# Optimization experiments

Measured on AMD Instinct MI355X. Metric: run time of the kernel, lower is better.

## Reference

```python
import jax, jax.numpy as jnp
import numpy as np

NUM_HEADS = 8
EMBED_DIM = 128
HEAD_DIM = EMBED_DIM // NUM_HEADS  # 16
NB_FEATURES = EMBED_DIM            # 128
EPS = 1e-4


def _make_projection(nb_rows, nb_cols, rng):
    # gaussian_orthogonal_random_matrix with scaling=0
    blocks = []
    for _ in range(nb_rows // nb_cols):
        q, _ = np.linalg.qr(rng.standard_normal((nb_cols, nb_cols)))
        blocks.append(q.T)
    rem = nb_rows - (nb_rows // nb_cols) * nb_cols
    if rem > 0:
        q, _ = np.linalg.qr(rng.standard_normal((nb_cols, nb_cols)))
        blocks.append(q.T[:rem])
    final = np.concatenate(blocks, axis=0)
    mult = np.linalg.norm(rng.standard_normal((nb_rows, nb_cols)), axis=1)
    return (mult[:, None] * final).astype(np.float32)


def setup_inputs() -> dict:
    key = jax.random.key(0)
    ks = jax.random.split(key, 7)
    R, C, E = 8, 2048, EMBED_DIM
    s = 1.0 / np.sqrt(E)
    x = jax.random.normal(ks[0], (R, C, E), dtype=jnp.float32)
    Wq = jax.random.uniform(ks[1], (E, E), jnp.float32, -s, s)
    bq = jax.random.uniform(ks[2], (E,), jnp.float32, -s, s)
    Wk = jax.random.uniform(ks[3], (E, E), jnp.float32, -s, s)
    bk = jax.random.uniform(ks[4], (E,), jnp.float32, -s, s)
    Wv = jax.random.uniform(ks[5], (E, E), jnp.float32, -s, s)
    bv = jax.random.uniform(ks[6], (E,), jnp.float32, -s, s)
    proj = jnp.asarray(_make_projection(NB_FEATURES, HEAD_DIM, np.random.default_rng(0)))
    return {"x": x, "Wq": Wq, "bq": bq, "Wk": Wk, "bk": bk, "Wv": Wv, "bv": bv, "proj": proj}


def _softmax_kernel(data, proj, is_query):
    # data: (R, h, n, d); proj: (F, d)
    d = data.shape[-1]
    normalizer = d ** (-0.25)
    ratio = proj.shape[0] ** (-0.5)
    data_dash = jnp.einsum('rhnd,jd->rhnj', normalizer * data, proj)  # (R,h,n,F)
    diag = jnp.sum(data * data, axis=-1, keepdims=True) * 0.5 * normalizer ** 2
    if is_query:
        m = jnp.max(data_dash, axis=-1, keepdims=True)
    else:
        m = jnp.max(data_dash, axis=(-1, -2), keepdims=True)
    return ratio * (jnp.exp(data_dash - diag - m) + EPS)


def reference(x, Wq, bq, Wk, bk, Wv, bv, proj):
    R, C, E = x.shape
    h, hd = NUM_HEADS, HEAD_DIM

    def proj_heads(W, b):
        y = jnp.einsum('rce,fe->rcf', x, W) + b
        return y.reshape(R, C, h, hd).transpose(0, 2, 1, 3)  # (R,h,C,hd)

    q = _softmax_kernel(proj_heads(Wq, bq), proj, is_query=True)   # (R,h,C,F)
    k = _softmax_kernel(proj_heads(Wk, bk), proj, is_query=False)  # (R,h,C,F)
    v = proj_heads(Wv, bv)                                          # (R,h,C,hd)

    # fold batch (R) into the feature dim: (h, C, R*F) / (h, C, R*hd)
    qf = q.transpose(1, 2, 0, 3).reshape(h, C, R * NB_FEATURES)
    kf = k.transpose(1, 2, 0, 3).reshape(h, C, R * NB_FEATURES)
    vf = v.transpose(1, 2, 0, 3).reshape(h, C, R * hd)

    k_sum = kf.sum(axis=-2)                                   # (h, D)
    D_inv = 1.0 / jnp.einsum('hnd,hd->hn', qf, k_sum)         # (h, C)
    context = jnp.einsum('hnd,hne->hde', kf, vf)              # (h, D, Ev)
    out = jnp.einsum('hde,hnd,hn->hne', context, qf, D_inv)   # (h, C, R*hd)

    out = out.reshape(h, C, R, hd).transpose(2, 1, 0, 3).reshape(R, C, E)
    attn = jnp.einsum('hqf,hkf->hqk', qf, kf)                 # (h, C, C)
    return out, attn
```

## Files before the change

kernel.cpp:

```cpp
#include <hip/hip_runtime.h>
#include <hip/hip_bf16.h>
#include <stdint.h>

typedef __bf16 bf16x8 __attribute__((ext_vector_type(8)));
typedef __bf16 bf16x4 __attribute__((ext_vector_type(4)));
typedef float  f32x4  __attribute__((ext_vector_type(4)));

#define RATIO 0.08838834764831845f
#define EPSV  1e-4f

#define GLOBAL_AS __attribute__((address_space(1)))
#define LDS_AS    __attribute__((address_space(3)))

static __device__ __forceinline__ void gload16(const void* g, void* l) {
  __builtin_amdgcn_global_load_lds((GLOBAL_AS const void*)g, (LDS_AS void*)l, 16, 0, 0);
}

static constexpr size_t OFF_XB    = 0;
static constexpr size_t OFF_WCAT  = OFF_XB    + 4194304;
static constexpr size_t OFF_MQ    = OFF_WCAT  + 98304;
static constexpr size_t OFF_MK    = OFF_MQ    + 262144;
static constexpr size_t OFF_BCAT  = OFF_MK    + 262144;
static constexpr size_t OFF_BQF   = OFF_BCAT  + 2048;
static constexpr size_t OFF_BKF   = OFF_BQF   + 4096;
static constexpr size_t OFF_Y     = OFF_BKF   + 4096;
static constexpr size_t OFF_QF    = OFF_Y     + 25165824;
static constexpr size_t OFF_KF    = OFF_QF    + 33554432;
static constexpr size_t OFF_KFT   = OFF_KF    + 33554432;
static constexpr size_t OFF_VFT   = OFF_KFT   + 33554432;
static constexpr size_t OFF_KPART = OFF_VFT   + 4194304;
static constexpr size_t OFF_KMAX  = OFF_KPART + 4096;
static constexpr size_t OFF_KSPART= OFF_KMAX  + 1024;
static constexpr size_t OFF_DPART = OFF_KSPART+ 524288;
static constexpr size_t OFF_CTXP  = OFF_DPART + 524288;
static constexpr size_t OFF_CTXT  = OFF_CTXP  + 16777216;
static constexpr size_t WS_NEED   = OFF_CTXT  + 2097152;

static __device__ __forceinline__ void gemm_core(
    const __hip_bfloat16* __restrict__ A, const __hip_bfloat16* __restrict__ B,
    int lda, int ldb, int K, int tm, int tn,
    __bf16* As, __bf16* Bs, f32x4 acc[4][4]) {
  const int t    = threadIdx.x;
  const int w    = t >> 6;
  const int lane = t & 63;
  const int m_off = (w >> 1) << 6;
  const int n_off = (w & 1) << 6;
  const int r0 = t >> 2;
  const int kk = (t & 3) << 3;
  char* Asb = (char*)As + (w << 10);
  char* Bsb = (char*)Bs + (w << 10);
  const int frow = lane & 15;
  const int koff = (lane >> 4) << 3;
  for (int k0 = 0; k0 < K; k0 += 32) {
    const __hip_bfloat16* Ag = A + (size_t)(tm + r0) * lda + (k0 + kk);
    const __hip_bfloat16* Bg = B + (size_t)(tn + r0) * ldb + (k0 + kk);
    gload16(Ag, Asb);
    gload16(Ag + (size_t)64 * lda, Asb + 4096);
    gload16(Bg, Bsb);
    gload16(Bg + (size_t)64 * ldb, Bsb + 4096);
    __syncthreads();
    bf16x8 af[4], bfr[4];
#pragma unroll
    for (int mi = 0; mi < 4; ++mi)
      af[mi] = *(const bf16x8*)(As + ((m_off + mi * 16 + frow) << 5) + koff);
#pragma unroll
    for (int ni = 0; ni < 4; ++ni)
      bfr[ni] = *(const bf16x8*)(Bs + ((n_off + ni * 16 + frow) << 5) + koff);
#pragma unroll
    for (int mi = 0; mi < 4; ++mi)
#pragma unroll
      for (int ni = 0; ni < 4; ++ni)
        acc[mi][ni] = __builtin_amdgcn_mfma_f32_16x16x32_bf16(af[mi], bfr[ni], acc[mi][ni], 0, 0, 0);
    __syncthreads();
  }
}

#define ZERO_ACC(acc) do {                                   \
  _Pragma("unroll") for (int a_ = 0; a_ < 4; ++a_)           \
  _Pragma("unroll") for (int b_ = 0; b_ < 4; ++b_)           \
    acc[a_][b_] = (f32x4){0.f, 0.f, 0.f, 0.f};               \
} while (0)

__global__ void k_prep(const float* __restrict__ x,
                       const float* __restrict__ Wq, const float* __restrict__ bq,
                       const float* __restrict__ Wk, const float* __restrict__ bk,
                       const float* __restrict__ Wv, const float* __restrict__ bv,
                       const float* __restrict__ proj,
                       __hip_bfloat16* __restrict__ xb,
                       __hip_bfloat16* __restrict__ Wcat, float* __restrict__ bcat,
                       __hip_bfloat16* __restrict__ Mq, __hip_bfloat16* __restrict__ Mk,
                       float* __restrict__ bqf, float* __restrict__ bkf) {
  const int b = blockIdx.x, t = threadIdx.x;
  {
    int i = (b * 256 + t) * 4;
    f32x4 v = *(const f32x4*)(x + i);
#pragma unroll
    for (int j = 0; j < 4; ++j) xb[i + j] = __float2bfloat16(v[j]);
  }
  if (b < 1024) {
    int i = b * 256 + t;
    {
      int which = i >> 17;
      int rem = i & 131071;
      int hj = rem >> 7, e = rem & 127;
      int hh = hj >> 7, j = hj & 127;
      const float* W = which ? Wk : Wq;
      float s = 0.f;
#pragma unroll
      for (int u = 0; u < 16; ++u) s += proj[j * 16 + u] * W[(hh * 16 + u) * 128 + e];
      if (which) Mk[rem] = __float2bfloat16(0.5f * s);
      else       Mq[rem] = __float2bfloat16(0.5f * s);
    }
    if (i < 2048) {
      int which = i >> 10;
      int hj = i & 1023, hh = hj >> 7, j = hj & 127;
      const float* bb = which ? bk : bq;
      float s = 0.f;
#pragma unroll
      for (int u = 0; u < 16; ++u) s += proj[j * 16 + u] * bb[hh * 16 + u];
      if (which) bkf[hj] = 0.5f * s;
      else       bqf[hj] = 0.5f * s;
    }
  }
  if (b < 192) {
    int i = b * 256 + t;
    int mat = i >> 14, rem = i & 16383;
    const float* W = (mat == 0) ? Wq : ((mat == 1) ? Wk : Wv);
    Wcat[i] = __float2bfloat16(W[rem]);
    if (i < 384) {
      int m2 = i >> 7;
      const float* bb = (m2 == 0) ? bq : ((m2 == 1) ? bk : bv);
      bcat[i] = bb[i & 127];
    }
  }
}

__global__ __launch_bounds__(256) void k_proj(
    const __hip_bfloat16* __restrict__ xb, const __hip_bfloat16* __restrict__ Wcat,
    const float* __restrict__ bcat, float* __restrict__ Y,
    __hip_bfloat16* __restrict__ vfT) {
  __shared__ __align__(16) char pool[34816];
  __bf16* As = (__bf16*)pool;
  __bf16* Bs = (__bf16*)(pool + 8192);
  const int tm = blockIdx.x << 7, tn = blockIdx.y << 7;
  f32x4 acc[4][4];
  ZERO_ACC(acc);
  gemm_core(xb, Wcat, 128, 128, 128, tm, tn, As, Bs, acc);
  const int t = threadIdx.x, w = t >> 6, lane = t & 63;
  const int m_off = (w >> 1) << 6, n_off = (w & 1) << 6;
  const int frow = lane & 15;
  if (tn == 256) {
    __bf16* vT = (__bf16*)pool;
#pragma unroll
    for (int ni = 0; ni < 4; ++ni) {
      const int j = n_off + ni * 16 + frow;
      const float bias = bcat[256 + j];
#pragma unroll
      for (int mi = 0; mi < 4; ++mi)
#pragma unroll
        for (int i = 0; i < 4; ++i) {
          const int rl = m_off + mi * 16 + ((lane >> 4) << 2) + i;
          vT[j * 136 + rl] = (__bf16)(acc[mi][ni][i] + bias);
        }
    }
    __syncthreads();
    const int r = tm >> 11, c0 = tm & 2047;
    const int j2 = t >> 1, half = t & 1;
    const int hh = j2 >> 4, aa = j2 & 15;
    __bf16* dst = (__bf16*)vfT + (((size_t)(hh * 128 + r * 16 + aa)) << 11) + c0 + (half << 6);
    const __bf16* srcr = vT + j2 * 136 + (half << 6);
#pragma unroll
    for (int q8 = 0; q8 < 8; ++q8)
      *(bf16x8*)(dst + (q8 << 3)) = *(const bf16x8*)(srcr + (q8 << 3));
  } else {
#pragma unroll
    for (int ni = 0; ni < 4; ++ni) {
      const int col = tn + n_off + ni * 16 + frow;
      const float bias = bcat[col];
#pragma unroll
      for (int mi = 0; mi < 4; ++mi)
#pragma unroll
        for (int i = 0; i < 4; ++i) {
          const int row = tm + m_off + mi * 16 + ((lane >> 4) << 2) + i;
          Y[(size_t)row * 384 + col] = acc[mi][ni][i] + bias;
        }
    }
  }
}

__global__ __launch_bounds__(256) void k_dashk_max(
    const __hip_bfloat16* __restrict__ xb, const __hip_bfloat16* __restrict__ Mk,
    const float* __restrict__ bkf, float* __restrict__ kpart) {
  __shared__ __align__(16) __bf16 As[4096], Bs[4096];
  __shared__ float wmax[4];
  const int h = blockIdx.y;
  const int tm = blockIdx.x << 7;
  f32x4 acc[4][4];
  ZERO_ACC(acc);
  gemm_core(xb, Mk + h * 16384, 128, 128, 128, tm, 0, As, Bs, acc);
  const int t = threadIdx.x, w = t >> 6, lane = t & 63;
  const int n_off = (w & 1) << 6;
  float mx = -1e30f;
#pragma unroll
  for (int ni = 0; ni < 4; ++ni) {
    const float bia = bkf[h * 128 + n_off + ni * 16 + (lane & 15)];
#pragma unroll
    for (int mi = 0; mi < 4; ++mi)
#pragma unroll
      for (int i = 0; i < 4; ++i) mx = fmaxf(mx, acc[mi][ni][i] + bia);
  }
#pragma unroll
  for (int off = 1; off < 64; off <<= 1) mx = fmaxf(mx, __shfl_xor(mx, off));
  if (lane == 0) wmax[w] = mx;
  __syncthreads();
  if (t == 0) kpart[h * 128 + blockIdx.x] = fmaxf(fmaxf(wmax[0], wmax[1]), fmaxf(wmax[2], wmax[3]));
}

__global__ __launch_bounds__(256) void k_dashk_feat(
    const __hip_bfloat16* __restrict__ xb, const __hip_bfloat16* __restrict__ Mk,
    const float* __restrict__ bkf, const float* __restrict__ Y,
    const float* __restrict__ kpart,
    __hip_bfloat16* __restrict__ kf, __hip_bfloat16* __restrict__ kfT,
    float* __restrict__ kspart) {
  __shared__ __align__(16) __bf16 As[4096], Bs[4096];
  __shared__ float diag_s[128];
  __shared__ __align__(16) __bf16 kT[128 * 136];
  __shared__ float ksp_s[2][128];
  const int h = blockIdx.y;
  const int tm = blockIdx.x << 7;
  f32x4 acc[4][4];
  ZERO_ACC(acc);
  gemm_core(xb, Mk + h * 16384, 128, 128, 128, tm, 0, As, Bs, acc);
  const int t = threadIdx.x, w = t >> 6, lane = t & 63;
  const int m_off = (w >> 1) << 6, n_off = (w & 1) << 6;
  const int frow = lane & 15;
  if (t < 128) {
    const float* yp = Y + (size_t)(tm + t) * 384 + 128 + h * 16;
    float s = 0.f;
#pragma unroll
    for (int u = 0; u < 16; ++u) s += yp[u] * yp[u];
    diag_s[t] = 0.125f * s;
  }
  const int r = tm >> 11;
  const int c0 = tm & 2047;
  const int cb = blockIdx.x & 15;
  float m = -1e30f;
  {
    const float* kp = kpart + h * 128 + r * 16;
#pragma unroll
    for (int i = 0; i < 16; ++i) m = fmaxf(m, kp[i]);
  }
  float bia[4];
#pragma unroll
  for (int ni = 0; ni < 4; ++ni) bia[ni] = bkf[h * 128 + n_off + ni * 16 + frow];
  float ksp[4] = {0.f, 0.f, 0.f, 0.f};
  __syncthreads();
#pragma unroll
  for (int mi = 0; mi < 4; ++mi) {
#pragma unroll
    for (int i = 0; i < 4; ++i) {
      const int rl = m_off + mi * 16 + ((lane >> 4) << 2) + i;
      const int c = c0 + rl;
      const float dm = diag_s[rl] + m;
#pragma unroll
      for (int ni = 0; ni < 4; ++ni) {
        const int j = n_off + ni * 16 + frow;
        const float f = RATIO * (__expf(acc[mi][ni][i] + bia[ni] - dm) + EPSV);
        const __hip_bfloat16 hb = __float2bfloat16(f);
        kf[((size_t)((h << 11) + c) << 10) + (r << 7) + j] = hb;
        kT[j * 136 + rl] = (__bf16)f;
        ksp[ni] += __bfloat162float(hb);
      }
    }
  }
#pragma unroll
  for (int ni = 0; ni < 4; ++ni) {
    ksp[ni] += __shfl_xor(ksp[ni], 16);
    ksp[ni] += __shfl_xor(ksp[ni], 32);
  }
  if ((lane >> 4) == 0) {
#pragma unroll
    for (int ni = 0; ni < 4; ++ni)
      ksp_s[w >> 1][n_off + ni * 16 + frow] = ksp[ni];
  }
  __syncthreads();
  if (t < 128)
    kspart[(((cb << 3) + h) << 10) + r * 128 + t] = ksp_s[0][t] + ksp_s[1][t];
  const int j2 = t >> 1, half = t & 1;
  __bf16* dst = (__bf16*)kfT + (((size_t)(h << 10) + (r << 7) + j2) << 11) + c0 + (half << 6);
  const __bf16* srcr = kT + j2 * 136 + (half << 6);
#pragma unroll
  for (int q8 = 0; q8 < 8; ++q8)
    *(bf16x8*)(dst + (q8 << 3)) = *(const bf16x8*)(srcr + (q8 << 3));
}

__global__ __launch_bounds__(256) void k_dashq(
    const __hip_bfloat16* __restrict__ xb, const __hip_bfloat16* __restrict__ Mq,
    const float* __restrict__ bqf, const float* __restrict__ Y,
    const float* __restrict__ kspart,
    __hip_bfloat16* __restrict__ qf, float* __restrict__ dpart) {
  __shared__ __align__(16) __bf16 As[4096], Bs[4096];
  __shared__ float diag_s[128];
  __shared__ float rmax_s[2][128];
  __shared__ float ksum_s[128];
  __shared__ float dred_s[2][128];
  const int h = blockIdx.y;
  const int tm = blockIdx.x << 7;
  const int r = tm >> 11, c0 = tm & 2047;
  f32x4 acc[4][4];
  ZERO_ACC(acc);
  const int t = threadIdx.x, w = t >> 6, lane = t & 63;
  if (t < 128) {
    const float* yp = Y + (size_t)(tm + t) * 384 + h * 16;
    float s = 0.f;
#pragma unroll
    for (int u = 0; u < 16; ++u) s += yp[u] * yp[u];
    diag_s[t] = 0.125f * s;
    float ks = 0.f;
#pragma unroll
    for (int cb = 0; cb < 16; ++cb) ks += kspart[(((cb << 3) + h) << 10) + r * 128 + t];
    ksum_s[t] = ks;
  }
  gemm_core(xb, Mq + h * 16384, 128, 128, 128, tm, 0, As, Bs, acc);
  const int m_off = (w >> 1) << 6, n_off = (w & 1) << 6;
  const int frow = lane & 15;
  float bia[4];
#pragma unroll
  for (int ni = 0; ni < 4; ++ni) bia[ni] = bqf[h * 128 + n_off + ni * 16 + frow];
  float rmx[4][4];
#pragma unroll
  for (int mi = 0; mi < 4; ++mi)
#pragma unroll
    for (int i = 0; i < 4; ++i) {
      float m0 = acc[mi][0][i] + bia[0];
      m0 = fmaxf(m0, acc[mi][1][i] + bia[1]);
      m0 = fmaxf(m0, acc[mi][2][i] + bia[2]);
      m0 = fmaxf(m0, acc[mi][3][i] + bia[3]);
      rmx[mi][i] = m0;
    }
#pragma unroll
  for (int off = 1; off < 16; off <<= 1)
#pragma unroll
    for (int mi = 0; mi < 4; ++mi)
#pragma unroll
      for (int i = 0; i < 4; ++i)
        rmx[mi][i] = fmaxf(rmx[mi][i], __shfl_xor(rmx[mi][i], off));
  if (frow == 0) {
#pragma unroll
    for (int mi = 0; mi < 4; ++mi)
#pragma unroll
      for (int i = 0; i < 4; ++i)
        rmax_s[w & 1][m_off + mi * 16 + ((lane >> 4) << 2) + i] = rmx[mi][i];
  }
  __syncthreads();
  float p[4][4];
#pragma unroll
  for (int mi = 0; mi < 4; ++mi)
#pragma unroll
    for (int i = 0; i < 4; ++i) p[mi][i] = 0.f;
#pragma unroll
  for (int mi = 0; mi < 4; ++mi) {
#pragma unroll
    for (int i = 0; i < 4; ++i) {
      const int rl = m_off + mi * 16 + ((lane >> 4) << 2) + i;
      const float md = diag_s[rl] + fmaxf(rmax_s[0][rl], rmax_s[1][rl]);
#pragma unroll
      for (int ni = 0; ni < 4; ++ni) {
        const int j = n_off + ni * 16 + frow;
        const float f = RATIO * (__expf(acc[mi][ni][i] + bia[ni] - md) + EPSV);
        const __hip_bfloat16 hb = __float2bfloat16(f);
        qf[((size_t)((h << 11) + c0 + rl) << 10) + (r << 7) + j] = hb;
        p[mi][i] += __bfloat162float(hb) * ksum_s[j];
      }
    }
  }
#pragma unroll
  for (int off = 1; off < 16; off <<= 1)
#pragma unroll
    for (int mi = 0; mi < 4; ++mi)
#pragma unroll
      for (int i = 0; i < 4; ++i)
        p[mi][i] += __shfl_xor(p[mi][i], off);
  if (frow == 0) {
#pragma unroll
    for (int mi = 0; mi < 4; ++mi)
#pragma unroll
      for (int i = 0; i < 4; ++i)
        dred_s[w & 1][m_off + mi * 16 + ((lane >> 4) << 2) + i] = p[mi][i];
  }
  __syncthreads();
  if (t < 128)
    dpart[(((r << 3) + h) << 11) + c0 + t] = dred_s[0][t] + dred_s[1][t];
}

#define SBAR() __builtin_amdgcn_s_barrier()
#define FEN()  do { asm volatile("" ::: "memory"); __builtin_amdgcn_sched_barrier(0); } while (0)
#define PRIO1() __builtin_amdgcn_s_setprio(1)
#define PRIO0() __builtin_amdgcn_s_setprio(0)
#define VMW4() do { asm volatile("s_waitcnt vmcnt(4)" ::: "memory"); } while (0)
#define VMW0() do { asm volatile("s_waitcnt vmcnt(0)" ::: "memory"); } while (0)

#define MFMA16(nlo) do {                                                      \
  _Pragma("unroll") for (int mi_ = 0; mi_ < 8; ++mi_)                         \
  _Pragma("unroll") for (int nj_ = 0; nj_ < 2; ++nj_)                         \
    acc[mi_][(nlo) + nj_] = __builtin_amdgcn_mfma_f32_16x16x32_bf16(          \
        aR[mi_], bR[nj_], acc[mi_][(nlo) + nj_], 0, 0, 0);                    \
} while (0)

__global__ __launch_bounds__(512, 2) void k_attn8(
    const __hip_bfloat16* __restrict__ qf, const __hip_bfloat16* __restrict__ kf,
    float* __restrict__ attn) {
  extern __shared__ __align__(128) char lds[];
  const int lid = blockIdx.x;
  const int swz = ((lid & 7) << 6) + (lid >> 3);
  const int h  = swz >> 6;
  const int tm = ((swz >> 3) & 7) << 8;
  const int tn = (swz & 7) << 8;
  const __hip_bfloat16* Ag = qf + ((size_t)h << 21);
  const __hip_bfloat16* Bg = kf + ((size_t)h << 21);

  const int t = threadIdx.x, wid = t >> 6, lane = t & 63;
  const int f = lane & 15;
  const int wr = wid >> 2, wc = wid & 3;
  const int swzg = (((lane >> 4) ^ ((f >> 1) & 3)) << 4);
  const int aoff = ((wr << 7) + f) * 64 + swzg;
  const int boff = 65536 + ((wc << 6) + f) * 64 + swzg;
  const int srow = t >> 2;
  const int scol = (((t & 3) ^ ((t >> 3) & 3)) << 3);
  const int sdst = wid << 10;

  f32x4 acc[8][4] = {};
  bf16x8 aR[8], bR[2];

  auto stageA = [&](int buf, int kh, int k0) {
    char* d = lds + buf * 32768 + kh * 16384 + sdst;
    const __hip_bfloat16* g = Ag + (size_t)(tm + srow) * 1024 + k0 + (kh << 5) + scol;
    gload16(g, d);
    gload16(g + 128 * 1024, d + 8192);
  };
  auto stageB = [&](int buf, int kh, int k0) {
    char* d = lds + 65536 + buf * 32768 + kh * 16384 + sdst;
    const __hip_bfloat16* g = Bg + (size_t)(tn + srow) * 1024 + k0 + (kh << 5) + scol;
    gload16(g, d);
    gload16(g + 128 * 1024, d + 8192);
  };

  stageA(0, 0, 0); stageB(0, 0, 0); stageA(0, 1, 0); stageB(0, 1, 0);
  VMW4();
  SBAR(); FEN();

  for (int kt = 0; kt < 15; ++kt) {
    const int buf = kt & 1, nbuf = buf ^ 1;
    const int bo = buf * 32768;
    const int nk0 = (kt + 1) << 6;
#pragma unroll
    for (int mi = 0; mi < 8; ++mi) aR[mi] = *(const bf16x8*)(lds + bo + aoff + mi * 1024);
    bR[0] = *(const bf16x8*)(lds + bo + boff);
    bR[1] = *(const bf16x8*)(lds + bo + boff + 1024);
    stageA(nbuf, 0, nk0);
    PRIO1(); MFMA16(0); PRIO0();
    bR[0] = *(const bf16x8*)(lds + bo + boff + 2048);
    bR[1] = *(const bf16x8*)(lds + bo + boff + 3072);
    stageB(nbuf, 0, nk0);
    PRIO1(); MFMA16(2); PRIO0();
    VMW4();
    SBAR(); FEN();
#pragma unroll
    for (int mi = 0; mi < 8; ++mi) aR[mi] = *(const bf16x8*)(lds + bo + 16384 + aoff + mi * 1024);
    bR[0] = *(const bf16x8*)(lds + bo + 16384 + boff);
    bR[1] = *(const bf16x8*)(lds + bo + 16384 + boff + 1024);
    stageA(nbuf, 1, nk0);
    PRIO1(); MFMA16(0); PRIO0();
    bR[0] = *(const bf16x8*)(lds + bo + 16384 + boff + 2048);
    bR[1] = *(const bf16x8*)(lds + bo + 16384 + boff + 3072);
    stageB(nbuf, 1, nk0);
    PRIO1(); MFMA16(2); PRIO0();
    VMW4();
    SBAR(); FEN();
  }
  {
    const int bo = 32768;
#pragma unroll
    for (int mi = 0; mi < 8; ++mi) aR[mi] = *(const bf16x8*)(lds + bo + aoff + mi * 1024);
    bR[0] = *(const bf16x8*)(lds + bo + boff);
    bR[1] = *(const bf16x8*)(lds + bo + boff + 1024);
    PRIO1(); MFMA16(0); PRIO0();
    bR[0] = *(const bf16x8*)(lds + bo + boff + 2048);
    bR[1] = *(const bf16x8*)(lds + bo + boff + 3072);
    PRIO1(); MFMA16(2); PRIO0();
    VMW0();
    SBAR(); FEN();
#pragma unroll
    for (int mi = 0; mi < 8; ++mi) aR[mi] = *(const bf16x8*)(lds + bo + 16384 + aoff + mi * 1024);
    bR[0] = *(const bf16x8*)(lds + bo + 16384 + boff);
    bR[1] = *(const bf16x8*)(lds + bo + 16384 + boff + 1024);
    PRIO1(); MFMA16(0); PRIO0();
    bR[0] = *(const bf16x8*)(lds + bo + 16384 + boff + 2048);
    bR[1] = *(const bf16x8*)(lds + bo + 16384 + boff + 3072);
    PRIO1(); MFMA16(2); PRIO0();
  }

  float* Cc = attn + ((size_t)h << 22);
  const int rbase = tm + (wr << 7) + ((lane >> 4) << 2);
  const int cbase = tn + (wc << 6) + f;
#pragma unroll
  for (int mi = 0; mi < 8; ++mi)
#pragma unroll
    for (int i = 0; i < 4; ++i) {
      float* rp = Cc + ((size_t)(rbase + mi * 16 + i) << 11) + cbase;
#pragma unroll
      for (int ni = 0; ni < 4; ++ni) rp[ni * 16] = acc[mi][ni][i];
    }
}

__global__ __launch_bounds__(256) void k_ctx(
    const __hip_bfloat16* __restrict__ vfT, const __hip_bfloat16* __restrict__ kfT,
    float* __restrict__ ctxp) {
  __shared__ __align__(16) __bf16 As[4096], Bs[4096];
  const int z = blockIdx.z, h = z >> 2, kc = z & 3;
  const int tn = blockIdx.y << 7;
  f32x4 acc[4][4];
  ZERO_ACC(acc);
  gemm_core(vfT + ((size_t)h << 18) + (kc << 9), kfT + ((size_t)h << 21) + (kc << 9),
            2048, 2048, 512, 0, tn, As, Bs, acc);
  float* Cp = ctxp + ((size_t)(kc * 8 + h) << 17);
  const int t = threadIdx.x, w = t >> 6, lane = t & 63;
  const int m_off = (w >> 1) << 6, n_off = (w & 1) << 6;
#pragma unroll
  for (int mi = 0; mi < 4; ++mi)
#pragma unroll
    for (int i = 0; i < 4; ++i) {
      const int row = m_off + mi * 16 + ((lane >> 4) << 2) + i;
#pragma unroll
      for (int ni = 0; ni < 4; ++ni) {
        const int col = tn + n_off + ni * 16 + (lane & 15);
        Cp[((size_t)row << 10) + col] = acc[mi][ni][i];
      }
    }
}

__global__ void k_ctxred(const float* __restrict__ ctxp, __hip_bfloat16* __restrict__ ctxT) {
  const int i = (blockIdx.x * 256 + threadIdx.x) * 4;
  f32x4 a = *(const f32x4*)(ctxp + i);
  f32x4 b = *(const f32x4*)(ctxp + i + 1048576);
  f32x4 c = *(const f32x4*)(ctxp + i + 2097152);
  f32x4 d = *(const f32x4*)(ctxp + i + 3145728);
  bf16x4 o;
#pragma unroll
  for (int j = 0; j < 4; ++j) o[j] = (__bf16)(a[j] + b[j] + c[j] + d[j]);
  *(bf16x4*)((__bf16*)ctxT + i) = o;
}

__global__ __launch_bounds__(256) void k_out64(
    const __hip_bfloat16* __restrict__ qf, const __hip_bfloat16* __restrict__ ctxT,
    const float* __restrict__ dpart, float* __restrict__ outp) {
  __shared__ __align__(16) __bf16 As[2048], Bs[4096];
  __shared__ float dinv_s[64];
  const int h = blockIdx.z;
  const int tm = blockIdx.x << 6;
  const int t = threadIdx.x, w = t >> 6, lane = t & 63;
  if (t < 64) {
    float s = 0.f;
#pragma unroll
    for (int r = 0; r < 8; ++r) s += dpart[(((r << 3) + h) << 11) + tm + t];
    dinv_s[t] = 1.0f / s;
  }
  const int m_off = (w >> 1) << 5, n_off = (w & 1) << 6;
  const int r0 = t >> 2, kk = (t & 3) << 3;
  char* Asb = (char*)As + ((t >> 6) << 10);
  char* Bsb = (char*)Bs + ((t >> 6) << 10);
  const int frow = lane & 15, koff = (lane >> 4) << 3;
  const __hip_bfloat16* A = qf + ((size_t)h << 21);
  const __hip_bfloat16* B = ctxT + ((size_t)h << 17);
  f32x4 acc[2][4];
#pragma unroll
  for (int a_ = 0; a_ < 2; ++a_)
#pragma unroll
    for (int b_ = 0; b_ < 4; ++b_) acc[a_][b_] = (f32x4){0.f, 0.f, 0.f, 0.f};
  for (int k0 = 0; k0 < 1024; k0 += 32) {
    const __hip_bfloat16* Agp = A + (size_t)(tm + r0) * 1024 + (k0 + kk);
    const __hip_bfloat16* Bgp = B + (size_t)r0 * 1024 + (k0 + kk);
    gload16(Agp, Asb);
    gload16(Bgp, Bsb);
    gload16(Bgp + (size_t)64 * 1024, Bsb + 4096);
    __syncthreads();
    bf16x8 af[2], bfr[4];
#pragma unroll
    for (int mi = 0; mi < 2; ++mi)
      af[mi] = *(const bf16x8*)(As + ((m_off + mi * 16 + frow) << 5) + koff);
#pragma unroll
    for (int ni = 0; ni < 4; ++ni)
      bfr[ni] = *(const bf16x8*)(Bs + ((n_off + ni * 16 + frow) << 5) + koff);
#pragma unroll
    for (int mi = 0; mi < 2; ++mi)
#pragma unroll
      for (int ni = 0; ni < 4; ++ni)
        acc[mi][ni] = __builtin_amdgcn_mfma_f32_16x16x32_bf16(af[mi], bfr[ni], acc[mi][ni], 0, 0, 0);
    __syncthreads();
  }
#pragma unroll
  for (int mi = 0; mi < 2; ++mi)
#pragma unroll
    for (int i = 0; i < 4; ++i) {
      const int rl = m_off + mi * 16 + ((lane >> 4) << 2) + i;
      const int row = tm + rl;
      const float dv = dinv_s[rl];
#pragma unroll
      for (int ni = 0; ni < 4; ++ni) {
        const int col = n_off + ni * 16 + frow;
        const int rb = col >> 4, tt = col & 15;
        outp[(((size_t)(rb << 11) + row) << 7) + (h << 4) + tt] = acc[mi][ni][i] * dv;
      }
    }
}

extern "C" void kernel_launch(void* const* d_in, const int* in_sizes, int n_in,
                              void* d_out, int out_size, void* d_ws, size_t ws_size,
                              hipStream_t stream) {
  const float* x    = (const float*)d_in[0];
  const float* Wq   = (const float*)d_in[1];
  const float* bq   = (const float*)d_in[2];
  const float* Wk   = (const float*)d_in[3];
  const float* bk   = (const float*)d_in[4];
  const float* Wv   = (const float*)d_in[5];
  const float* bv   = (const float*)d_in[6];
  const float* proj = (const float*)d_in[7];
  if (ws_size < WS_NEED) return;

  char* ws = (char*)d_ws;
  __hip_bfloat16* xb   = (__hip_bfloat16*)(ws + OFF_XB);
  __hip_bfloat16* Wcat = (__hip_bfloat16*)(ws + OFF_WCAT);
  __hip_bfloat16* Mq   = (__hip_bfloat16*)(ws + OFF_MQ);
  __hip_bfloat16* Mk   = (__hip_bfloat16*)(ws + OFF_MK);
  float* bcat = (float*)(ws + OFF_BCAT);
  float* bqf  = (float*)(ws + OFF_BQF);
  float* bkf  = (float*)(ws + OFF_BKF);
  float* Y    = (float*)(ws + OFF_Y);
  __hip_bfloat16* qf  = (__hip_bfloat16*)(ws + OFF_QF);
  __hip_bfloat16* kf  = (__hip_bfloat16*)(ws + OFF_KF);
  __hip_bfloat16* kfT = (__hip_bfloat16*)(ws + OFF_KFT);
  __hip_bfloat16* vfT = (__hip_bfloat16*)(ws + OFF_VFT);
  float* kpart  = (float*)(ws + OFF_KPART);
  float* kspart = (float*)(ws + OFF_KSPART);
  float* dpart  = (float*)(ws + OFF_DPART);
  float* ctxp   = (float*)(ws + OFF_CTXP);
  __hip_bfloat16* ctxT = (__hip_bfloat16*)(ws + OFF_CTXT);

  float* outp = (float*)d_out;
  float* attn = (float*)d_out + 2097152;

  static int attr_done = 0;
  if (!attr_done) {
    (void)hipFuncSetAttribute((const void*)k_attn8,
                              hipFuncAttributeMaxDynamicSharedMemorySize, 131072);
    attr_done = 1;
  }

  k_prep<<<dim3(2048), dim3(256), 0, stream>>>(x, Wq, bq, Wk, bk, Wv, bv, proj,
                                               xb, Wcat, bcat, Mq, Mk, bqf, bkf);
  k_proj<<<dim3(128, 3), dim3(256), 0, stream>>>(xb, Wcat, bcat, Y, vfT);
  k_dashk_max<<<dim3(128, 8), dim3(256), 0, stream>>>(xb, Mk, bkf, kpart);
  k_dashk_feat<<<dim3(128, 8), dim3(256), 0, stream>>>(xb, Mk, bkf, Y, kpart, kf, kfT, kspart);
  k_dashq<<<dim3(128, 8), dim3(256), 0, stream>>>(xb, Mq, bqf, Y, kspart, qf, dpart);
  k_attn8<<<dim3(512), dim3(512), 131072, stream>>>(qf, kf, attn);
  k_ctx<<<dim3(1, 8, 32), dim3(256), 0, stream>>>(vfT, kfT, ctxp);
  k_ctxred<<<dim3(1024), dim3(256), 0, stream>>>(ctxp, ctxT);
  k_out64<<<dim3(32, 1, 8), dim3(256), 0, stream>>>(qf, ctxT, dpart, outp);
}
```

Measured before the change: 183.6 us.

## Fuse key max and feature kernels into one cooperative grid-synced kernel

Replaces the two-pass key feature computation (one kernel computing per-block maxima, then a second recomputing the GEMM to produce features) with a single cooperative kernel. It computes the GEMM once, reduces the block maximum with an order-preserving integer atomicMax, syncs the grid, then applies the exponential and writes kf, kfT and the partial sums. This removes the duplicated GEMM and one launch, at the cost of needing all 1024 blocks resident at once, plus a grid barrier. If the cooperative launch fails it falls back to the original two kernels.

```diff
diff --git a/kernel.cpp b/kernel.cpp
--- a/kernel.cpp
+++ b/kernel.cpp
@@ -1,6 +1,9 @@
 #include <hip/hip_runtime.h>
 #include <hip/hip_bf16.h>
+#include <hip/hip_cooperative_groups.h>
 #include <stdint.h>
+
+namespace cg = cooperative_groups;
 
 typedef __bf16 bf16x8 __attribute__((ext_vector_type(8)));
 typedef __bf16 bf16x4 __attribute__((ext_vector_type(4)));
@@ -14,6 +17,15 @@
 
 static __device__ __forceinline__ void gload16(const void* g, void* l) {
   __builtin_amdgcn_global_load_lds((GLOBAL_AS const void*)g, (LDS_AS void*)l, 16, 0, 0);
+}
+
+static __device__ __forceinline__ unsigned fkey(float f) {
+  unsigned b = __float_as_uint(f);
+  return (b & 0x80000000u) ? ~b : (b | 0x80000000u);
+}
+static __device__ __forceinline__ float funkey(unsigned k) {
+  unsigned b = (k & 0x80000000u) ? (k & 0x7FFFFFFFu) : ~k;
+  return __uint_as_float(b);
 }
 
 static constexpr size_t OFF_XB    = 0;
@@ -89,7 +101,8 @@
                        __hip_bfloat16* __restrict__ xb,
                        __hip_bfloat16* __restrict__ Wcat, float* __restrict__ bcat,
                        __hip_bfloat16* __restrict__ Mq, __hip_bfloat16* __restrict__ Mk,
-                       float* __restrict__ bqf, float* __restrict__ bkf) {
+                       float* __restrict__ bqf, float* __restrict__ bkf,
+                       unsigned* __restrict__ kmaxI) {
   const int b = blockIdx.x, t = threadIdx.x;
   {
     int i = (b * 256 + t) * 4;
@@ -97,6 +110,7 @@
 #pragma unroll
     for (int j = 0; j < 4; ++j) xb[i + j] = __float2bfloat16(v[j]);
   }
+  if (b == 0 && t < 64) kmaxI[t] = 0u;
   if (b < 1024) {
     int i = b * 256 + t;
     {
@@ -186,6 +200,100 @@
         }
     }
   }
+}
+
+__global__ __launch_bounds__(256, 4) void k_dashk_coop(
+    const __hip_bfloat16* __restrict__ xb, const __hip_bfloat16* __restrict__ Mk,
+    const float* __restrict__ bkf, const float* __restrict__ Y,
+    unsigned* __restrict__ kmaxI,
+    __hip_bfloat16* __restrict__ kf, __hip_bfloat16* __restrict__ kfT,
+    float* __restrict__ kspart) {
+  __shared__ __align__(16) char pool[34816];
+  __shared__ float diag_s[128];
+  __shared__ float wmax_s[4];
+  __shared__ float m_s;
+  __shared__ float ksp_s[2][128];
+  __bf16* As = (__bf16*)pool;
+  __bf16* Bs = (__bf16*)(pool + 8192);
+  __bf16* kT = (__bf16*)pool;
+  const int h = blockIdx.y;
+  const int tm = blockIdx.x << 7;
+  const int t = threadIdx.x, w = t >> 6, lane = t & 63;
+  if (t < 128) {
+    const float* yp = Y + (size_t)(tm + t) * 384 + 128 + h * 16;
+    float s = 0.f;
+#pragma unroll
+    for (int u = 0; u < 16; ++u) s += yp[u] * yp[u];
+    diag_s[t] = 0.125f * s;
+  }
+  f32x4 acc[4][4];
+  ZERO_ACC(acc);
+  gemm_core(xb, Mk + h * 16384, 128, 128, 128, tm, 0, As, Bs, acc);
+  const int m_off = (w >> 1) << 6, n_off = (w & 1) << 6;
+  const int frow = lane & 15;
+  const int r = tm >> 11;
+  const int c0 = tm & 2047;
+  const int cb = blockIdx.x & 15;
+  float bia[4];
+#pragma unroll
+  for (int ni = 0; ni < 4; ++ni) bia[ni] = bkf[h * 128 + n_off + ni * 16 + frow];
+  float mx = -1e30f;
+#pragma unroll
+  for (int ni = 0; ni < 4; ++ni)
+#pragma unroll
+    for (int mi = 0; mi < 4; ++mi)
+#pragma unroll
+      for (int i = 0; i < 4; ++i) mx = fmaxf(mx, acc[mi][ni][i] + bia[ni]);
+#pragma unroll
+  for (int off = 1; off < 64; off <<= 1) mx = fmaxf(mx, __shfl_xor(mx, off));
+  if (lane == 0) wmax_s[w] = mx;
+  __syncthreads();
+  if (t == 0) {
+    float bm = fmaxf(fmaxf(wmax_s[0], wmax_s[1]), fmaxf(wmax_s[2], wmax_s[3]));
+    atomicMax(&kmaxI[r * 8 + h], fkey(bm));
+  }
+  cg::this_grid().sync();
+  if (t == 0) m_s = funkey(atomicMax(&kmaxI[r * 8 + h], 0u));
+  __syncthreads();
+  const float m = m_s;
+  float ksp[4] = {0.f, 0.f, 0.f, 0.f};
+#pragma unroll
+  for (int mi = 0; mi < 4; ++mi) {
+#pragma unroll
+    for (int i = 0; i < 4; ++i) {
+      const int rl = m_off + mi * 16 + ((lane >> 4) << 2) + i;
+      const int c = c0 + rl;
+      const float dm = diag_s[rl] + m;
+#pragma unroll
+      for (int ni = 0; ni < 4; ++ni) {
+        const int j = n_off + ni * 16 + frow;
+        const float f = RATIO * (__expf(acc[mi][ni][i] + bia[ni] - dm) + EPSV);
+        const __hip_bfloat16 hb = __float2bfloat16(f);
+        kf[((size_t)((h << 11) + c) << 10) + (r << 7) + j] = hb;
+        kT[j * 136 + rl] = (__bf16)f;
+        ksp[ni] += __bfloat162float(hb);
+      }
+    }
+  }
+#pragma unroll
+  for (int ni = 0; ni < 4; ++ni) {
+    ksp[ni] += __shfl_xor(ksp[ni], 16);
+    ksp[ni] += __shfl_xor(ksp[ni], 32);
+  }
+  if ((lane >> 4) == 0) {
+#pragma unroll
+    for (int ni = 0; ni < 4; ++ni)
+      ksp_s[w >> 1][n_off + ni * 16 + frow] = ksp[ni];
+  }
+  __syncthreads();
+  if (t < 128)
+    kspart[(((cb << 3) + h) << 10) + r * 128 + t] = ksp_s[0][t] + ksp_s[1][t];
+  const int j2 = t >> 1, half = t & 1;
+  __bf16* dst = (__bf16*)kfT + (((size_t)(h << 10) + (r << 7) + j2) << 11) + c0 + (half << 6);
+  const __bf16* srcr = kT + j2 * 136 + (half << 6);
+#pragma unroll
+  for (int q8 = 0; q8 < 8; ++q8)
+    *(bf16x8*)(dst + (q8 << 3)) = *(const bf16x8*)(srcr + (q8 << 3));
 }
 
 __global__ __launch_bounds__(256) void k_dashk_max(
@@ -641,6 +749,7 @@
   __hip_bfloat16* kfT = (__hip_bfloat16*)(ws + OFF_KFT);
   __hip_bfloat16* vfT = (__hip_bfloat16*)(ws + OFF_VFT);
   float* kpart  = (float*)(ws + OFF_KPART);
+  unsigned* kmaxI = (unsigned*)(ws + OFF_KMAX);
   float* kspart = (float*)(ws + OFF_KSPART);
   float* dpart  = (float*)(ws + OFF_DPART);
   float* ctxp   = (float*)(ws + OFF_CTXP);
@@ -657,10 +766,19 @@
   }
 
   k_prep<<<dim3(2048), dim3(256), 0, stream>>>(x, Wq, bq, Wk, bk, Wv, bv, proj,
-                                               xb, Wcat, bcat, Mq, Mk, bqf, bkf);
+                                               xb, Wcat, bcat, Mq, Mk, bqf, bkf, kmaxI);
   k_proj<<<dim3(128, 3), dim3(256), 0, stream>>>(xb, Wcat, bcat, Y, vfT);
-  k_dashk_max<<<dim3(128, 8), dim3(256), 0, stream>>>(xb, Mk, bkf, kpart);
-  k_dashk_feat<<<dim3(128, 8), dim3(256), 0, stream>>>(xb, Mk, bkf, Y, kpart, kf, kfT, kspart);
+  {
+    void* args[] = {(void*)&xb, (void*)&Mk, (void*)&bkf, (void*)&Y,
+                    (void*)&kmaxI, (void*)&kf, (void*)&kfT, (void*)&kspart};
+    hipError_t e = hipLaunchCooperativeKernel((void*)k_dashk_coop, dim3(128, 8),
+                                              dim3(256), args, 0, stream);
+    if (e != hipSuccess) {
+      (void)hipGetLastError();
+      k_dashk_max<<<dim3(128, 8), dim3(256), 0, stream>>>(xb, Mk, bkf, kpart);
+      k_dashk_feat<<<dim3(128, 8), dim3(256), 0, stream>>>(xb, Mk, bkf, Y, kpart, kf, kfT, kspart);
+    }
+  }
   k_dashq<<<dim3(128, 8), dim3(256), 0, stream>>>(xb, Mq, bqf, Y, kspart, qf, dpart);
   k_attn8<<<dim3(512), dim3(512), 131072, stream>>>(qf, kf, attn);
   k_ctx<<<dim3(1, 8, 32), dim3(256), 0, stream>>>(vfT, kfT, ctxp);
```

New measurement: 302.1 us. 64.5% more time.

## Load full K=128 tiles into swizzled LDS in one pass for projection GEMMs

Applied to the files above, without the earlier changes.

Adds a GEMM core that stages the whole 128x128 A and B tiles (K=128) into LDS at once, with an XOR swizzle to avoid bank conflicts, replacing the old loop of 32-wide K slices with a barrier pair per step. All four projection/feature kernels use it, and k_dashk_feat reuses the staging pool for its transpose buffer. This cuts barrier count and load/compute serialization. In exchange each block needs about 64KB of LDS, which lowers occupancy per CU.

```diff
diff --git a/kernel.cpp b/kernel.cpp
--- a/kernel.cpp
+++ b/kernel.cpp
@@ -75,6 +75,50 @@
   }
 }
 
+static __device__ __forceinline__ void gemm_core_k128(
+    const __hip_bfloat16* __restrict__ A, const __hip_bfloat16* __restrict__ B,
+    int lda, int ldb, int tm, int tn,
+    __bf16* As, __bf16* Bs, f32x4 acc[4][4]) {
+  const int t = threadIdx.x, w = t >> 6, lane = t & 63;
+  const int m_off = (w >> 1) << 6, n_off = (w & 1) << 6;
+  const int frow = lane & 15;
+  const int g0 = lane >> 4;
+  const int srow = (w << 5) + (lane >> 4);
+  const int sg = lane & 15;
+  char* Ab = (char*)As + (w << 13);
+  char* Bb = (char*)Bs + (w << 13);
+#pragma unroll
+  for (int j = 0; j < 8; ++j) {
+    const int row = srow + (j << 2);
+    const int scol = (sg ^ (row & 15)) << 3;
+    gload16(A + (size_t)(tm + row) * lda + scol, Ab + (j << 10));
+    gload16(B + (size_t)(tn + row) * ldb + scol, Bb + (j << 10));
+  }
+  __syncthreads();
+#pragma unroll
+  for (int kk = 0; kk < 4; ++kk) {
+    bf16x8 af[4], bfr[4];
+#pragma unroll
+    for (int mi = 0; mi < 4; ++mi) {
+      const int row = m_off + mi * 16 + frow;
+      const int gr = ((kk << 2) + g0) ^ (row & 15);
+      af[mi] = *(const bf16x8*)((char*)As + row * 256 + gr * 16);
+    }
+#pragma unroll
+    for (int ni = 0; ni < 4; ++ni) {
+      const int row = n_off + ni * 16 + frow;
+      const int gr = ((kk << 2) + g0) ^ (row & 15);
+      bfr[ni] = *(const bf16x8*)((char*)Bs + row * 256 + gr * 16);
+    }
+#pragma unroll
+    for (int mi = 0; mi < 4; ++mi)
+#pragma unroll
+      for (int ni = 0; ni < 4; ++ni)
+        acc[mi][ni] = __builtin_amdgcn_mfma_f32_16x16x32_bf16(af[mi], bfr[ni], acc[mi][ni], 0, 0, 0);
+  }
+  __syncthreads();
+}
+
 #define ZERO_ACC(acc) do {                                   \
   _Pragma("unroll") for (int a_ = 0; a_ < 4; ++a_)           \
   _Pragma("unroll") for (int b_ = 0; b_ < 4; ++b_)           \
@@ -139,13 +183,13 @@
     const __hip_bfloat16* __restrict__ xb, const __hip_bfloat16* __restrict__ Wcat,
     const float* __restrict__ bcat, float* __restrict__ Y,
     __hip_bfloat16* __restrict__ vfT) {
-  __shared__ __align__(16) char pool[34816];
+  __shared__ __align__(16) char pool[65536];
   __bf16* As = (__bf16*)pool;
-  __bf16* Bs = (__bf16*)(pool + 8192);
+  __bf16* Bs = (__bf16*)(pool + 32768);
   const int tm = blockIdx.x << 7, tn = blockIdx.y << 7;
   f32x4 acc[4][4];
   ZERO_ACC(acc);
-  gemm_core(xb, Wcat, 128, 128, 128, tm, tn, As, Bs, acc);
+  gemm_core_k128(xb, Wcat, 128, 128, tm, tn, As, Bs, acc);
   const int t = threadIdx.x, w = t >> 6, lane = t & 63;
   const int m_off = (w >> 1) << 6, n_off = (w & 1) << 6;
   const int frow = lane & 15;
@@ -191,13 +235,15 @@
 __global__ __launch_bounds__(256) void k_dashk_max(
     const __hip_bfloat16* __restrict__ xb, const __hip_bfloat16* __restrict__ Mk,
     const float* __restrict__ bkf, float* __restrict__ kpart) {
-  __shared__ __align__(16) __bf16 As[4096], Bs[4096];
+  __shared__ __align__(16) char pool[65536];
   __shared__ float wmax[4];
+  __bf16* As = (__bf16*)pool;
+  __bf16* Bs = (__bf16*)(pool + 32768);
   const int h = blockIdx.y;
   const int tm = blockIdx.x << 7;
   f32x4 acc[4][4];
   ZERO_ACC(acc);
-  gemm_core(xb, Mk + h * 16384, 128, 128, 128, tm, 0, As, Bs, acc);
+  gemm_core_k128(xb, Mk + h * 16384, 128, 128, tm, 0, As, Bs, acc);
   const int t = threadIdx.x, w = t >> 6, lane = t & 63;
   const int n_off = (w & 1) << 6;
   float mx = -1e30f;
@@ -222,18 +268,15 @@
     const float* __restrict__ kpart,
     __hip_bfloat16* __restrict__ kf, __hip_bfloat16* __restrict__ kfT,
     float* __restrict__ kspart) {
-  __shared__ __align__(16) __bf16 As[4096], Bs[4096];
+  __shared__ __align__(16) char pool[65536];
   __shared__ float diag_s[128];
-  __shared__ __align__(16) __bf16 kT[128 * 136];
   __shared__ float ksp_s[2][128];
+  __bf16* As = (__bf16*)pool;
+  __bf16* Bs = (__bf16*)(pool + 32768);
+  __bf16* kT = (__bf16*)pool;
   const int h = blockIdx.y;
   const int tm = blockIdx.x << 7;
-  f32x4 acc[4][4];
-  ZERO_ACC(acc);
-  gemm_core(xb, Mk + h * 16384, 128, 128, 128, tm, 0, As, Bs, acc);
   const int t = threadIdx.x, w = t >> 6, lane = t & 63;
-  const int m_off = (w >> 1) << 6, n_off = (w & 1) << 6;
-  const int frow = lane & 15;
   if (t < 128) {
     const float* yp = Y + (size_t)(tm + t) * 384 + 128 + h * 16;
     float s = 0.f;
@@ -241,6 +284,11 @@
     for (int u = 0; u < 16; ++u) s += yp[u] * yp[u];
     diag_s[t] = 0.125f * s;
   }
+  f32x4 acc[4][4];
+  ZERO_ACC(acc);
+  gemm_core_k128(xb, Mk + h * 16384, 128, 128, tm, 0, As, Bs, acc);
+  const int m_off = (w >> 1) << 6, n_off = (w & 1) << 6;
+  const int frow = lane & 15;
   const int r = tm >> 11;
   const int c0 = tm & 2047;
   const int cb = blockIdx.x & 15;
@@ -254,7 +302,6 @@
 #pragma unroll
   for (int ni = 0; ni < 4; ++ni) bia[ni] = bkf[h * 128 + n_off + ni * 16 + frow];
   float ksp[4] = {0.f, 0.f, 0.f, 0.f};
-  __syncthreads();
 #pragma unroll
   for (int mi = 0; mi < 4; ++mi) {
 #pragma unroll
@@ -299,11 +346,13 @@
     const float* __restrict__ bqf, const float* __restrict__ Y,
     const float* __restrict__ kspart,
     __hip_bfloat16* __restrict__ qf, float* __restrict__ dpart) {
-  __shared__ __align__(16) __bf16 As[4096], Bs[4096];
+  __shared__ __align__(16) char pool[65536];
   __shared__ float diag_s[128];
   __shared__ float rmax_s[2][128];
   __shared__ float ksum_s[128];
   __shared__ float dred_s[2][128];
+  __bf16* As = (__bf16*)pool;
+  __bf16* Bs = (__bf16*)(pool + 32768);
   const int h = blockIdx.y;
   const int tm = blockIdx.x << 7;
   const int r = tm >> 11, c0 = tm & 2047;
@@ -321,7 +370,7 @@
     for (int cb = 0; cb < 16; ++cb) ks += kspart[(((cb << 3) + h) << 10) + r * 128 + t];
     ksum_s[t] = ks;
   }
-  gemm_core(xb, Mq + h * 16384, 128, 128, 128, tm, 0, As, Bs, acc);
+  gemm_core_k128(xb, Mq + h * 16384, 128, 128, tm, 0, As, Bs, acc);
   const int m_off = (w >> 1) << 6, n_off = (w & 1) << 6;
   const int frow = lane & 15;
   float bia[4];
```

Result: no change. 183.8 us (median of 2 runs) (+0.1%).
